# Kernel optimization log

Hardware: AMD Instinct MI355X
Metric: run time of the kernel (lower is better)

The kernel has to match this reference:

```python
import jax, jax.numpy as jnp
import numpy as np

N = 8192
IN_DIM = 256
HID = 256
OUT_DIM = 256
P_DIM = 3
SIGMA = 1.0


def setup_inputs() -> dict:
    key = jax.random.key(0)
    ks = jax.random.split(key, 7)
    s_in = 1.0 / np.sqrt(IN_DIM)
    inp = {
        "X": jax.random.normal(ks[0], (N, IN_DIM + P_DIM), dtype=jnp.float32),
        "WQ": jax.random.uniform(ks[1], (IN_DIM, HID), jnp.float32, -s_in, s_in),
        "bQ": jax.random.uniform(ks[2], (HID,), jnp.float32, -s_in, s_in),
        "WK": jax.random.uniform(ks[3], (IN_DIM, HID), jnp.float32, -s_in, s_in),
        "bK": jax.random.uniform(ks[4], (HID,), jnp.float32, -s_in, s_in),
        "WV": jax.random.uniform(ks[5], (IN_DIM, OUT_DIM), jnp.float32, -s_in, s_in),
        "bV": jax.random.uniform(ks[6], (OUT_DIM,), jnp.float32, -s_in, s_in),
    }
    return inp


def _softmax_one(x):
    # exp(x - max) / (1 + sum(exp(x - max))) -- faithful to the torch softmax_one
    m = jnp.max(x, axis=-1, keepdims=True)
    e = jnp.exp(x - m)
    return e / (1.0 + jnp.sum(e, axis=-1, keepdims=True))


def reference(X, WQ, bQ, WK, bK, WV, bV):
    P = X[:, -P_DIM:]            # [N, 3] spatial coords
    Xf = X[:, :-P_DIM]           # [N, IN_DIM] features

    Q = Xf @ WQ + bQ             # [N, HID]
    K = Xf @ WK + bK             # [N, HID]
    V = Xf @ WV + bV             # [N, OUT_DIM]

    scores = (Q @ K.T) / jnp.sqrt(jnp.asarray(HID, Xf.dtype))  # [N, N]

    # squared pairwise distances ||P_i - P_j||^2 (cdist(P,P)**2)
    sq = jnp.sum(P * P, axis=-1)                                # [N]
    d2 = jnp.maximum(sq[:, None] + sq[None, :] - 2.0 * (P @ P.T), 0.0)
    decay = jnp.exp(-d2 / (2.0 * SIGMA ** 2))                   # [N, N]

    A = _softmax_one(scores * decay)                             # [N, N]
    H = A @ V                                                    # [N, OUT_DIM]
    # residual: input_dim == output_dim so res_proj is None
    return H + Xf
```

## Files before the change

kernel.cpp:

```cpp
#include <hip/hip_runtime.h>
#include <hip/hip_bf16.h>
#include <stdint.h>

#define NTOK 8192
#define XSTRIDE 259
#define LOG2E 1.4426950408889634f
#define DECC (-3.4712336270551023f)
#define KSPLIT 8
#define SPLEN (NTOK / KSPLIT)
#define BN 32
#define ITERS (SPLEN / BN)

typedef __bf16 bf16x8 __attribute__((ext_vector_type(8)));
typedef float f32x4 __attribute__((ext_vector_type(4)));
typedef float f32x16 __attribute__((ext_vector_type(16)));
typedef unsigned short u16;

union BF8 { u16 u[8]; bf16x8 v; };
union PW  { uint32_t u[4]; bf16x8 v; };

__device__ __forceinline__ u16 f2bf(float f) {
  uint32_t u = __float_as_uint(f);
  u += 0x7FFFu + ((u >> 16) & 1u);
  return (u16)(u >> 16);
}
__device__ __forceinline__ float bf2f(u16 h) {
  return __uint_as_float(((uint32_t)h) << 16);
}
__device__ __forceinline__ float exp2_hw(float x) {
  float r; asm("v_exp_f32 %0, %1" : "=v"(r) : "v"(x)); return r;
}
__device__ __forceinline__ f32x4 mfma16(bf16x8 a, bf16x8 b, f32x4 c) {
  return __builtin_amdgcn_mfma_f32_16x16x32_bf16(a, b, c, 0, 0, 0);
}
__device__ __forceinline__ f32x16 mfma32(bf16x8 a, bf16x8 b, f32x16 c) {
  return __builtin_amdgcn_mfma_f32_32x32x16_bf16(a, b, c, 0, 0, 0);
}
__device__ __forceinline__ void async16(const void* g, void* l) {
  __builtin_amdgcn_global_load_lds(
      (const __attribute__((address_space(1))) uint32_t*)g,
      (__attribute__((address_space(3))) uint32_t*)l, 16, 0, 0);
}
__device__ __forceinline__ void bsplit(float v, u16& h, u16& l) {
  h = f2bf(v);
  l = f2bf(v - bf2f(h));
}

__global__ __launch_bounds__(256) void pos_kernel(
    const float* __restrict__ X, u16* __restrict__ Qp, u16* __restrict__ Kp) {
  const int r = blockIdx.x * 256 + threadIdx.x;
  const float* xp = X + (size_t)r * XSTRIDE + 256;
  const float x = xp[0], y = xp[1], z = xp[2];
  const float w = 0.5f * (x * x + y * y + z * z);
  u16 xh, xl, yh, yl, zh, zl, wh, wl;
  bsplit(x, xh, xl); bsplit(y, yh, yl); bsplit(z, zh, zl); bsplit(w, wh, wl);
  const u16 one = 0x3F80u;
  const u16 SGN = 0x8000u;
  union { u16 u[16]; uint4 v4[2]; } uq, uk;
  uq.u[0] = wh;  uk.u[0] = one;
  uq.u[1] = wl;  uk.u[1] = one;
  uq.u[2] = one; uk.u[2] = wh;
  uq.u[3] = one; uk.u[3] = wl;
  uq.u[4] = (u16)(xh ^ SGN); uk.u[4] = xh;
  uq.u[5] = (u16)(xh ^ SGN); uk.u[5] = xl;
  uq.u[6] = (u16)(xl ^ SGN); uk.u[6] = xh;
  uq.u[7] = (u16)(yh ^ SGN); uk.u[7] = yh;
  uq.u[8] = (u16)(yh ^ SGN); uk.u[8] = yl;
  uq.u[9] = (u16)(yl ^ SGN); uk.u[9] = yh;
  uq.u[10] = (u16)(zh ^ SGN); uk.u[10] = zh;
  uq.u[11] = (u16)(zh ^ SGN); uk.u[11] = zl;
  uq.u[12] = (u16)(zl ^ SGN); uk.u[12] = zh;
  uq.u[13] = 0; uk.u[13] = 0;
  uq.u[14] = 0; uk.u[14] = 0;
  uq.u[15] = 0; uk.u[15] = 0;
  ((uint4*)Qp)[r * 2] = uq.v4[0];
  ((uint4*)Qp)[r * 2 + 1] = uq.v4[1];
  ((uint4*)Kp)[r * 2] = uk.v4[0];
  ((uint4*)Kp)[r * 2 + 1] = uk.v4[1];
}

__global__ __launch_bounds__(256) void xb_kernel(
    const float* __restrict__ X, u16* __restrict__ Xb) {
  const int t = threadIdx.x;
  const int row = blockIdx.x * 8 + (t >> 5);
  const int c0 = (t & 31) * 8;
  const float* xp = X + (size_t)row * XSTRIDE + c0;
  union { u16 u[8]; uint4 v; } o;
#pragma unroll
  for (int j = 0; j < 8; ++j) o.u[j] = f2bf(xp[j]);
  *(uint4*)(Xb + (size_t)row * 256 + c0) = o.v;
}

__global__ __launch_bounds__(256) void wprep_kernel(
    const float* __restrict__ WQ, const float* __restrict__ WK,
    const float* __restrict__ WV, u16* __restrict__ Wt) {
  const int o = blockIdx.x;
  const int which = o >> 8, oo = o & 255;
  const float* W = (which == 0) ? WQ : ((which == 1) ? WK : WV);
  const int k = threadIdx.x;
  Wt[(size_t)o * 256 + k] = f2bf(W[(size_t)k * 256 + oo]);
}

__global__ __launch_bounds__(256) void qkv_kernel(
    const u16* __restrict__ Xb, const u16* __restrict__ Wt,
    const float* __restrict__ bQ, const float* __restrict__ bK,
    const float* __restrict__ bV,
    u16* __restrict__ Qb, u16* __restrict__ Kb, u16* __restrict__ Vt) {
  __shared__ u16 wt[64 * 256];
  const int tid = threadIdx.x;
  const int lane = tid & 63;
  const int wave = tid >> 6;
  const int l15 = lane & 15;
  const int q4 = lane >> 4;
  const int rb = blockIdx.x;
  const int ch = blockIdx.y;
  const int which = ch >> 2;
  const int c0 = (ch & 3) * 64;
  const float* bias = (which == 0) ? bQ : ((which == 1) ? bK : bV);

  bf16x8 xa[2][8];
#pragma unroll
  for (int mt = 0; mt < 2; ++mt) {
    const int row = rb * 128 + wave * 32 + mt * 16 + l15;
#pragma unroll
    for (int kc = 0; kc < 8; ++kc)
      xa[mt][kc] = *(const bf16x8*)(Xb + (size_t)row * 256 + kc * 32 + q4 * 8);
  }
  {
    const u16* Wsrc = Wt + (size_t)(which * 256 + c0) * 256;
    const int rb0 = wave * 16;
#pragma unroll
    for (int i = 0; i < 8; ++i) {
      int r = rb0 + i * 2 + (lane >> 5);
      int c = (lane & 31) ^ (r & 7);
      async16(Wsrc + (size_t)r * 256 + c * 8, wt + (rb0 + i * 2) * 256);
    }
  }
  asm volatile("s_waitcnt vmcnt(0)" ::: "memory");
  __syncthreads();

  f32x4 acc[2][4];
#pragma unroll
  for (int mt = 0; mt < 2; ++mt)
#pragma unroll
    for (int nt = 0; nt < 4; ++nt) acc[mt][nt] = (f32x4){0.f, 0.f, 0.f, 0.f};

#pragma unroll
  for (int kc = 0; kc < 8; ++kc) {
#pragma unroll
    for (int nt = 0; nt < 4; ++nt) {
      bf16x8 wf = *(const bf16x8*)(wt + (nt * 16 + l15) * 256 +
                                   (((kc * 4 + q4) ^ (l15 & 7)) * 8));
#pragma unroll
      for (int mt = 0; mt < 2; ++mt)
        acc[mt][nt] = mfma16(xa[mt][kc], wf, acc[mt][nt]);
    }
  }
  float bc[4];
#pragma unroll
  for (int nt = 0; nt < 4; ++nt) bc[nt] = bias[c0 + nt * 16 + l15];

#pragma unroll
  for (int mt = 0; mt < 2; ++mt)
#pragma unroll
    for (int nt = 0; nt < 4; ++nt)
#pragma unroll
      for (int r = 0; r < 4; ++r) {
        float v = acc[mt][nt][r] + bc[nt];
        int grow = rb * 128 + wave * 32 + mt * 16 + q4 * 4 + r;
        int gc = c0 + nt * 16 + l15;
        if (which == 2)      Vt[(size_t)gc * NTOK + grow] = f2bf(v);
        else if (which == 1) Kb[(size_t)grow * 256 + gc] = f2bf(v);
        else                 Qb[(size_t)((grow >> 5) * 16 + (gc >> 4)) * 512 +
                                ((gc >> 3) & 1) * 256 + (grow & 31) * 8 +
                                (gc & 7)] = f2bf(v);
      }
}

__global__ __launch_bounds__(512, 2) void attn_kernel(
    const u16* __restrict__ Qb, const u16* __restrict__ Kb,
    const u16* __restrict__ Vt, const u16* __restrict__ Qp,
    const u16* __restrict__ Kp, u16* __restrict__ Op,
    float* __restrict__ ml) {
  __shared__ u16 kbuf[3][BN * 256];
  __shared__ u16 vbuf[3][256 * BN];
  __shared__ u16 kpbuf[3][BN * 16];

  const int tid = threadIdx.x;
  const int lane = tid & 63;
  const int wave = tid >> 6;
  const int l31 = lane & 31;
  const int h5 = lane >> 5;
  const int sp = blockIdx.x;
  const int rb = blockIdx.y;
  const int q0 = rb * 256;
  const int wrow = wave * 32;

#define STAGE(T, S_)                                                          \
  do {                                                                        \
    const int key0_ = sp * SPLEN + (T) * BN;                                  \
    _Pragma("unroll")                                                         \
    for (int j = 0; j < 2; ++j) {                                             \
      int r = wave * 4 + j * 2 + (lane >> 5);                                 \
      int c = (lane & 31) ^ (r & 7);                                          \
      async16(Kb + (size_t)(key0_ + r) * 256 + c * 8,                         \
              &kbuf[S_][(wave * 4 + j * 2) * 256]);                           \
    }                                                                         \
    _Pragma("unroll")                                                         \
    for (int j = 0; j < 2; ++j) {                                             \
      int f = wave * 32 + j * 16 + (lane >> 2);                               \
      int c = (lane & 3) ^ ((f >> 1) & 3);                                    \
      async16(Vt + (size_t)f * NTOK + key0_ + c * 8,                          \
              &vbuf[S_][(wave * 32 + j * 16) * 32]);                          \
    }                                                                         \
    if (wave == 0)                                                            \
      async16(Kp + (size_t)(key0_ + (lane >> 1)) * 16 + (lane & 1) * 8,       \
              &kpbuf[S_][0]);                                                 \
  } while (0)

  const int rb32 = rb * 8 + wave;
  bf16x8 qa[16];
#pragma unroll
  for (int kc = 0; kc < 16; ++kc)
    qa[kc] = *(const bf16x8*)(Qb + ((size_t)(rb32 * 16 + kc) * 64 + lane) * 8);

  const bf16x8 qp = *(const bf16x8*)(Qp + (size_t)(q0 + wrow + l31) * 16 +
                                     h5 * 8);

  f32x16 O[8];
#pragma unroll
  for (int ft = 0; ft < 8; ++ft)
#pragma unroll
    for (int r = 0; r < 16; ++r) O[ft][r] = 0.f;
  float lrow = 0.f;

  const int kswz = l31 & 7;
  const int vswz = (l31 >> 1) & 3;

  STAGE(0, 0);
  STAGE(1, 1);

  int cur = 0;
#pragma unroll 1
  for (int t = 0; t < ITERS; ++t) {
    if (t + 1 < ITERS) {
      if (wave == 0) asm volatile("s_waitcnt vmcnt(5)" ::: "memory");
      else           asm volatile("s_waitcnt vmcnt(4)" ::: "memory");
    } else {
      asm volatile("s_waitcnt vmcnt(0)" ::: "memory");
    }
    __builtin_amdgcn_s_barrier();

    if (t + 2 < ITERS) {
      const int s2 = (cur >= 1) ? (cur - 1) : 2;
      STAGE(t + 2, s2);
    }

    f32x16 T;
#pragma unroll
    for (int r = 0; r < 16; ++r) T[r] = 0.f;
    {
      bf16x8 kpf = *(const bf16x8*)(&kpbuf[cur][l31 * 16 + h5 * 8]);
      T = mfma32(kpf, qp, T);
    }

    f32x16 S;
#pragma unroll
    for (int r = 0; r < 16; ++r) S[r] = 0.f;
    __builtin_amdgcn_s_setprio(1);
#pragma unroll
    for (int kc = 0; kc < 16; ++kc) {
      bf16x8 kf = *(const bf16x8*)(&kbuf[cur][l31 * 256 +
                                   (((2 * kc + h5) ^ kswz) * 8)]);
      S = mfma32(kf, qa[kc], S);
    }
    __builtin_amdgcn_s_setprio(0);

#pragma unroll
    for (int r = 0; r < 16; ++r) {
      float dec = exp2_hw(fmaf(T[r], -LOG2E, DECC));
      float p = exp2_hw(S[r] * dec);
      S[r] = p;
      lrow += p;
    }

    uint32_t w0, w1, w2, w3, w4, w5, w6, w7;
    asm("v_cvt_pk_bf16_f32 %0, %1, %2" : "=v"(w0) : "v"(S[0]),  "v"(S[1]));
    asm("v_cvt_pk_bf16_f32 %0, %1, %2" : "=v"(w1) : "v"(S[2]),  "v"(S[3]));
    asm("v_cvt_pk_bf16_f32 %0, %1, %2" : "=v"(w2) : "v"(S[4]),  "v"(S[5]));
    asm("v_cvt_pk_bf16_f32 %0, %1, %2" : "=v"(w3) : "v"(S[6]),  "v"(S[7]));
    asm("v_cvt_pk_bf16_f32 %0, %1, %2" : "=v"(w4) : "v"(S[8]),  "v"(S[9]));
    asm("v_cvt_pk_bf16_f32 %0, %1, %2" : "=v"(w5) : "v"(S[10]), "v"(S[11]));
    asm("v_cvt_pk_bf16_f32 %0, %1, %2" : "=v"(w6) : "v"(S[12]), "v"(S[13]));
    asm("v_cvt_pk_bf16_f32 %0, %1, %2" : "=v"(w7) : "v"(S[14]), "v"(S[15]));
    asm volatile("v_permlane32_swap_b32 %0, %1" : "+v"(w2), "+v"(w0));
    asm volatile("v_permlane32_swap_b32 %0, %1" : "+v"(w3), "+v"(w1));
    asm volatile("v_permlane32_swap_b32 %0, %1" : "+v"(w6), "+v"(w4));
    asm volatile("v_permlane32_swap_b32 %0, %1" : "+v"(w7), "+v"(w5));
    PW pa0, pa1;
    pa0.u[0] = w0; pa0.u[1] = w1; pa0.u[2] = w2; pa0.u[3] = w3;
    pa1.u[0] = w4; pa1.u[1] = w5; pa1.u[2] = w6; pa1.u[3] = w7;

    __builtin_amdgcn_s_setprio(1);
#pragma unroll
    for (int kh = 0; kh < 2; ++kh) {
      const bf16x8 pa = kh ? pa1.v : pa0.v;
#pragma unroll
      for (int ft = 0; ft < 8; ++ft) {
        bf16x8 vf = *(const bf16x8*)(&vbuf[cur][(ft * 32 + l31) * 32 +
                                     (((2 * kh + h5) ^ vswz) * 8)]);
        O[ft] = mfma32(pa, vf, O[ft]);
      }
    }
    __builtin_amdgcn_s_setprio(0);

    cur = (cur == 2) ? 0 : (cur + 1);
  }

  float lsum = lrow + __shfl_xor(lrow, 32);
#pragma unroll
  for (int ft = 0; ft < 8; ++ft)
#pragma unroll
    for (int r = 0; r < 16; ++r) {
      int row = q0 + wrow + (r & 3) + 8 * (r >> 2) + 4 * h5;
      Op[((size_t)sp * NTOK + row) * 256 + ft * 32 + l31] = f2bf(O[ft][r]);
    }
  if (lane < 32)
    ml[sp * NTOK + q0 + wrow + lane] = lsum;
#undef STAGE
}

__global__ __launch_bounds__(256) void combine_kernel(
    const float* __restrict__ X, const u16* __restrict__ Op,
    const float* __restrict__ ml, float* __restrict__ out) {
  const int row = blockIdx.x;
  const int f = threadIdx.x;
  float den = 1.f, num = 0.f;
#pragma unroll
  for (int s = 0; s < KSPLIT; ++s) {
    den += ml[s * NTOK + row];
    num += bf2f(Op[((size_t)s * NTOK + row) * 256 + f]);
  }
  out[(size_t)row * 256 + f] = num / den + X[(size_t)row * XSTRIDE + f];
}

extern "C" void kernel_launch(void* const* d_in, const int* in_sizes, int n_in,
                              void* d_out, int out_size, void* d_ws, size_t ws_size,
                              hipStream_t stream) {
  (void)in_sizes; (void)n_in; (void)out_size; (void)ws_size;
  const float* X  = (const float*)d_in[0];
  const float* WQ = (const float*)d_in[1];
  const float* bQ = (const float*)d_in[2];
  const float* WK = (const float*)d_in[3];
  const float* bK = (const float*)d_in[4];
  const float* WV = (const float*)d_in[5];
  const float* bV = (const float*)d_in[6];
  float* out = (float*)d_out;
  char* ws = (char*)d_ws;

  u16*   Qb = (u16*)(ws);
  u16*   Kb = (u16*)(ws + ((size_t)4 << 20));
  u16*   Vt = (u16*)(ws + ((size_t)8 << 20));
  u16*   Qp = (u16*)(ws + ((size_t)12 << 20));
  u16*   Kp = (u16*)(ws + ((size_t)12 << 20) + 262144);
  u16*   Wt = (u16*)(ws + ((size_t)12 << 20) + 524288);
  u16*   Xb = (u16*)(ws + ((size_t)12 << 20) + 524288 + 393216);
  float* ml = (float*)(ws + ((size_t)16 << 20) + 524288 + 393216);
  u16*   Op = (u16*)(ws + ((size_t)16 << 20) + 524288 + 393216 + 524288);

  pos_kernel<<<dim3(NTOK / 256), dim3(256), 0, stream>>>(X, Qp, Kp);
  xb_kernel<<<dim3(NTOK / 8), dim3(256), 0, stream>>>(X, Xb);
  wprep_kernel<<<dim3(768), dim3(256), 0, stream>>>(WQ, WK, WV, Wt);
  qkv_kernel<<<dim3(64, 12), dim3(256), 0, stream>>>(Xb, Wt, bQ, bK, bV,
                                                     Qb, Kb, Vt);
  attn_kernel<<<dim3(KSPLIT, NTOK / 256), dim3(512), 0, stream>>>(
      Qb, Kb, Vt, Qp, Kp, Op, ml);
  combine_kernel<<<dim3(NTOK), dim3(256), 0, stream>>>(X, Op, ml, out);
}
```

Before: 208.7 us.

## Double-buffer 64-key attention tiles, fuse pos prep, stage QKV stores through LDS

The attention loop moves from a triple-buffered 32-key pipeline to double-buffered 64-key tiles, each processed as two 32-key sub-steps. This halves the barrier count but waits for all loads with vmcnt(0) every iteration. The positional-encoding prep is folded into the bf16 conversion kernel to save a launch. QKV outputs are now staged through LDS so global stores are coalesced 16-byte writes, and the combine kernel processes two rows per block with paired loads and stores.

```diff
diff --git a/kernel.cpp b/kernel.cpp
--- a/kernel.cpp
+++ b/kernel.cpp
@@ -8,7 +8,7 @@
 #define DECC (-3.4712336270551023f)
 #define KSPLIT 8
 #define SPLEN (NTOK / KSPLIT)
-#define BN 32
+#define BN 64
 #define ITERS (SPLEN / BN)
 
 typedef __bf16 bf16x8 __attribute__((ext_vector_type(8)));
@@ -46,41 +46,9 @@
   l = f2bf(v - bf2f(h));
 }
 
-__global__ __launch_bounds__(256) void pos_kernel(
-    const float* __restrict__ X, u16* __restrict__ Qp, u16* __restrict__ Kp) {
-  const int r = blockIdx.x * 256 + threadIdx.x;
-  const float* xp = X + (size_t)r * XSTRIDE + 256;
-  const float x = xp[0], y = xp[1], z = xp[2];
-  const float w = 0.5f * (x * x + y * y + z * z);
-  u16 xh, xl, yh, yl, zh, zl, wh, wl;
-  bsplit(x, xh, xl); bsplit(y, yh, yl); bsplit(z, zh, zl); bsplit(w, wh, wl);
-  const u16 one = 0x3F80u;
-  const u16 SGN = 0x8000u;
-  union { u16 u[16]; uint4 v4[2]; } uq, uk;
-  uq.u[0] = wh;  uk.u[0] = one;
-  uq.u[1] = wl;  uk.u[1] = one;
-  uq.u[2] = one; uk.u[2] = wh;
-  uq.u[3] = one; uk.u[3] = wl;
-  uq.u[4] = (u16)(xh ^ SGN); uk.u[4] = xh;
-  uq.u[5] = (u16)(xh ^ SGN); uk.u[5] = xl;
-  uq.u[6] = (u16)(xl ^ SGN); uk.u[6] = xh;
-  uq.u[7] = (u16)(yh ^ SGN); uk.u[7] = yh;
-  uq.u[8] = (u16)(yh ^ SGN); uk.u[8] = yl;
-  uq.u[9] = (u16)(yl ^ SGN); uk.u[9] = yh;
-  uq.u[10] = (u16)(zh ^ SGN); uk.u[10] = zh;
-  uq.u[11] = (u16)(zh ^ SGN); uk.u[11] = zl;
-  uq.u[12] = (u16)(zl ^ SGN); uk.u[12] = zh;
-  uq.u[13] = 0; uk.u[13] = 0;
-  uq.u[14] = 0; uk.u[14] = 0;
-  uq.u[15] = 0; uk.u[15] = 0;
-  ((uint4*)Qp)[r * 2] = uq.v4[0];
-  ((uint4*)Qp)[r * 2 + 1] = uq.v4[1];
-  ((uint4*)Kp)[r * 2] = uk.v4[0];
-  ((uint4*)Kp)[r * 2 + 1] = uk.v4[1];
-}
-
 __global__ __launch_bounds__(256) void xb_kernel(
-    const float* __restrict__ X, u16* __restrict__ Xb) {
+    const float* __restrict__ X, u16* __restrict__ Xb,
+    u16* __restrict__ Qp, u16* __restrict__ Kp) {
   const int t = threadIdx.x;
   const int row = blockIdx.x * 8 + (t >> 5);
   const int c0 = (t & 31) * 8;
@@ -89,6 +57,38 @@
 #pragma unroll
   for (int j = 0; j < 8; ++j) o.u[j] = f2bf(xp[j]);
   *(uint4*)(Xb + (size_t)row * 256 + c0) = o.v;
+
+  if (t < 8) {
+    const int r = blockIdx.x * 8 + t;
+    const float* pp = X + (size_t)r * XSTRIDE + 256;
+    const float x = pp[0], y = pp[1], z = pp[2];
+    const float w = 0.5f * (x * x + y * y + z * z);
+    u16 xh, xl, yh, yl, zh, zl, wh, wl;
+    bsplit(x, xh, xl); bsplit(y, yh, yl); bsplit(z, zh, zl); bsplit(w, wh, wl);
+    const u16 one = 0x3F80u;
+    const u16 SGN = 0x8000u;
+    union { u16 u[16]; uint4 v4[2]; } uq, uk;
+    uq.u[0] = wh;  uk.u[0] = one;
+    uq.u[1] = wl;  uk.u[1] = one;
+    uq.u[2] = one; uk.u[2] = wh;
+    uq.u[3] = one; uk.u[3] = wl;
+    uq.u[4] = (u16)(xh ^ SGN); uk.u[4] = xh;
+    uq.u[5] = (u16)(xh ^ SGN); uk.u[5] = xl;
+    uq.u[6] = (u16)(xl ^ SGN); uk.u[6] = xh;
+    uq.u[7] = (u16)(yh ^ SGN); uk.u[7] = yh;
+    uq.u[8] = (u16)(yh ^ SGN); uk.u[8] = yl;
+    uq.u[9] = (u16)(yl ^ SGN); uk.u[9] = yh;
+    uq.u[10] = (u16)(zh ^ SGN); uk.u[10] = zh;
+    uq.u[11] = (u16)(zh ^ SGN); uk.u[11] = zl;
+    uq.u[12] = (u16)(zl ^ SGN); uk.u[12] = zh;
+    uq.u[13] = 0; uk.u[13] = 0;
+    uq.u[14] = 0; uk.u[14] = 0;
+    uq.u[15] = 0; uk.u[15] = 0;
+    ((uint4*)Qp)[r * 2] = uq.v4[0];
+    ((uint4*)Qp)[r * 2 + 1] = uq.v4[1];
+    ((uint4*)Kp)[r * 2] = uk.v4[0];
+    ((uint4*)Kp)[r * 2 + 1] = uk.v4[1];
+  }
 }
 
 __global__ __launch_bounds__(256) void wprep_kernel(
@@ -106,7 +106,7 @@
     const float* __restrict__ bQ, const float* __restrict__ bK,
     const float* __restrict__ bV,
     u16* __restrict__ Qb, u16* __restrict__ Kb, u16* __restrict__ Vt) {
-  __shared__ u16 wt[64 * 256];
+  __shared__ u16 smem[64 * 256];
   const int tid = threadIdx.x;
   const int lane = tid & 63;
   const int wave = tid >> 6;
@@ -133,7 +133,7 @@
     for (int i = 0; i < 8; ++i) {
       int r = rb0 + i * 2 + (lane >> 5);
       int c = (lane & 31) ^ (r & 7);
-      async16(Wsrc + (size_t)r * 256 + c * 8, wt + (rb0 + i * 2) * 256);
+      async16(Wsrc + (size_t)r * 256 + c * 8, smem + (rb0 + i * 2) * 256);
     }
   }
   asm volatile("s_waitcnt vmcnt(0)" ::: "memory");
@@ -149,7 +149,7 @@
   for (int kc = 0; kc < 8; ++kc) {
 #pragma unroll
     for (int nt = 0; nt < 4; ++nt) {
-      bf16x8 wf = *(const bf16x8*)(wt + (nt * 16 + l15) * 256 +
+      bf16x8 wf = *(const bf16x8*)(smem + (nt * 16 + l15) * 256 +
                                    (((kc * 4 + q4) ^ (l15 & 7)) * 8));
 #pragma unroll
       for (int mt = 0; mt < 2; ++mt)
@@ -160,21 +160,52 @@
 #pragma unroll
   for (int nt = 0; nt < 4; ++nt) bc[nt] = bias[c0 + nt * 16 + l15];
 
-#pragma unroll
-  for (int mt = 0; mt < 2; ++mt)
-#pragma unroll
-    for (int nt = 0; nt < 4; ++nt)
-#pragma unroll
-      for (int r = 0; r < 4; ++r) {
-        float v = acc[mt][nt][r] + bc[nt];
-        int grow = rb * 128 + wave * 32 + mt * 16 + q4 * 4 + r;
-        int gc = c0 + nt * 16 + l15;
-        if (which == 2)      Vt[(size_t)gc * NTOK + grow] = f2bf(v);
-        else if (which == 1) Kb[(size_t)grow * 256 + gc] = f2bf(v);
-        else                 Qb[(size_t)((grow >> 5) * 16 + (gc >> 4)) * 512 +
-                                ((gc >> 3) & 1) * 256 + (grow & 31) * 8 +
-                                (gc & 7)] = f2bf(v);
+  __syncthreads();
+  const int grow0 = rb * 128;
+
+  if (which == 2) {
+#pragma unroll
+    for (int mt = 0; mt < 2; ++mt)
+#pragma unroll
+      for (int nt = 0; nt < 4; ++nt) {
+        const int lcol = nt * 16 + l15;
+        const int lrow0 = wave * 32 + mt * 16 + q4 * 4;
+        union { u16 u[4]; uint2 w; } p;
+#pragma unroll
+        for (int r = 0; r < 4; ++r) p.u[r] = f2bf(acc[mt][nt][r] + bc[nt]);
+        *(uint2*)(smem + lcol * 136 + lrow0) = p.w;
       }
+    __syncthreads();
+#pragma unroll
+    for (int i = 0; i < 4; ++i) {
+      int chn = i * 256 + tid;
+      int lcol = chn >> 4, s = chn & 15;
+      uint4 d = *(const uint4*)(smem + lcol * 136 + s * 8);
+      *(uint4*)(Vt + (size_t)(c0 + lcol) * NTOK + grow0 + s * 8) = d;
+    }
+  } else {
+#pragma unroll
+    for (int mt = 0; mt < 2; ++mt)
+#pragma unroll
+      for (int nt = 0; nt < 4; ++nt)
+#pragma unroll
+        for (int r = 0; r < 4; ++r)
+          smem[(wave * 32 + mt * 16 + q4 * 4 + r) * 72 + nt * 16 + l15] =
+              f2bf(acc[mt][nt][r] + bc[nt]);
+    __syncthreads();
+#pragma unroll
+    for (int i = 0; i < 4; ++i) {
+      int chn = i * 256 + tid;
+      int lrow = chn >> 3, g = chn & 7;
+      uint4 d = *(const uint4*)(smem + lrow * 72 + g * 8);
+      int grow = grow0 + lrow, gc = c0 + g * 8;
+      if (which == 1)
+        *(uint4*)(Kb + (size_t)grow * 256 + gc) = d;
+      else
+        *(uint4*)(Qb + (size_t)((grow >> 5) * 16 + (gc >> 4)) * 512 +
+                  ((gc >> 3) & 1) * 256 + (grow & 31) * 8) = d;
+    }
+  }
 }
 
 __global__ __launch_bounds__(512, 2) void attn_kernel(
@@ -182,9 +213,9 @@
     const u16* __restrict__ Vt, const u16* __restrict__ Qp,
     const u16* __restrict__ Kp, u16* __restrict__ Op,
     float* __restrict__ ml) {
-  __shared__ u16 kbuf[3][BN * 256];
-  __shared__ u16 vbuf[3][256 * BN];
-  __shared__ u16 kpbuf[3][BN * 16];
+  __shared__ u16 kbuf[2][BN * 256];
+  __shared__ u16 vbuf[2][256 * BN];
+  __shared__ u16 kpbuf[2][BN * 16];
 
   const int tid = threadIdx.x;
   const int lane = tid & 63;
@@ -200,22 +231,26 @@
   do {                                                                        \
     const int key0_ = sp * SPLEN + (T) * BN;                                  \
     _Pragma("unroll")                                                         \
-    for (int j = 0; j < 2; ++j) {                                             \
-      int r = wave * 4 + j * 2 + (lane >> 5);                                 \
+    for (int j = 0; j < 4; ++j) {                                             \
+      int r = wave * 8 + j * 2 + (lane >> 5);                                 \
       int c = (lane & 31) ^ (r & 7);                                          \
       async16(Kb + (size_t)(key0_ + r) * 256 + c * 8,                         \
-              &kbuf[S_][(wave * 4 + j * 2) * 256]);                           \
+              &kbuf[S_][(wave * 8 + j * 2) * 256]);                           \
     }                                                                         \
     _Pragma("unroll")                                                         \
-    for (int j = 0; j < 2; ++j) {                                             \
-      int f = wave * 32 + j * 16 + (lane >> 2);                               \
-      int c = (lane & 3) ^ ((f >> 1) & 3);                                    \
+    for (int j = 0; j < 4; ++j) {                                             \
+      int f = wave * 32 + j * 8 + (lane >> 3);                                \
+      int c = (lane & 7) ^ (f & 7);                                           \
       async16(Vt + (size_t)f * NTOK + key0_ + c * 8,                          \
-              &vbuf[S_][(wave * 32 + j * 16) * 32]);                          \
+              &vbuf[S_][(wave * 32 + j * 8) * BN]);                           \
     }                                                                         \
-    if (wave == 0)                                                            \
-      async16(Kp + (size_t)(key0_ + (lane >> 1)) * 16 + (lane & 1) * 8,       \
-              &kpbuf[S_][0]);                                                 \
+    if (wave == 0) {                                                          \
+      _Pragma("unroll")                                                       \
+      for (int hh = 0; hh < 2; ++hh)                                          \
+        async16(Kp + (size_t)(key0_ + hh * 32 + (lane >> 1)) * 16 +           \
+                    (lane & 1) * 8,                                           \
+                &kpbuf[S_][hh * 32 * 16]);                                    \
+    }                                                                         \
   } while (0)
 
   const int rb32 = rb * 8 + wave;
@@ -234,87 +269,79 @@
     for (int r = 0; r < 16; ++r) O[ft][r] = 0.f;
   float lrow = 0.f;
 
-  const int kswz = l31 & 7;
-  const int vswz = (l31 >> 1) & 3;
+  const int swz = l31 & 7;
 
   STAGE(0, 0);
-  STAGE(1, 1);
-
-  int cur = 0;
+
 #pragma unroll 1
   for (int t = 0; t < ITERS; ++t) {
-    if (t + 1 < ITERS) {
-      if (wave == 0) asm volatile("s_waitcnt vmcnt(5)" ::: "memory");
-      else           asm volatile("s_waitcnt vmcnt(4)" ::: "memory");
-    } else {
-      asm volatile("s_waitcnt vmcnt(0)" ::: "memory");
-    }
+    const int slot = t & 1;
+    asm volatile("s_waitcnt vmcnt(0)" ::: "memory");
     __builtin_amdgcn_s_barrier();
-
-    if (t + 2 < ITERS) {
-      const int s2 = (cur >= 1) ? (cur - 1) : 2;
-      STAGE(t + 2, s2);
-    }
-
-    f32x16 T;
-#pragma unroll
-    for (int r = 0; r < 16; ++r) T[r] = 0.f;
-    {
-      bf16x8 kpf = *(const bf16x8*)(&kpbuf[cur][l31 * 16 + h5 * 8]);
-      T = mfma32(kpf, qp, T);
-    }
-
-    f32x16 S;
-#pragma unroll
-    for (int r = 0; r < 16; ++r) S[r] = 0.f;
-    __builtin_amdgcn_s_setprio(1);
-#pragma unroll
-    for (int kc = 0; kc < 16; ++kc) {
-      bf16x8 kf = *(const bf16x8*)(&kbuf[cur][l31 * 256 +
-                                   (((2 * kc + h5) ^ kswz) * 8)]);
-      S = mfma32(kf, qa[kc], S);
-    }
-    __builtin_amdgcn_s_setprio(0);
-
-#pragma unroll
-    for (int r = 0; r < 16; ++r) {
-      float dec = exp2_hw(fmaf(T[r], -LOG2E, DECC));
-      float p = exp2_hw(S[r] * dec);
-      S[r] = p;
-      lrow += p;
-    }
-
-    uint32_t w0, w1, w2, w3, w4, w5, w6, w7;
-    asm("v_cvt_pk_bf16_f32 %0, %1, %2" : "=v"(w0) : "v"(S[0]),  "v"(S[1]));
-    asm("v_cvt_pk_bf16_f32 %0, %1, %2" : "=v"(w1) : "v"(S[2]),  "v"(S[3]));
-    asm("v_cvt_pk_bf16_f32 %0, %1, %2" : "=v"(w2) : "v"(S[4]),  "v"(S[5]));
-    asm("v_cvt_pk_bf16_f32 %0, %1, %2" : "=v"(w3) : "v"(S[6]),  "v"(S[7]));
-    asm("v_cvt_pk_bf16_f32 %0, %1, %2" : "=v"(w4) : "v"(S[8]),  "v"(S[9]));
-    asm("v_cvt_pk_bf16_f32 %0, %1, %2" : "=v"(w5) : "v"(S[10]), "v"(S[11]));
-    asm("v_cvt_pk_bf16_f32 %0, %1, %2" : "=v"(w6) : "v"(S[12]), "v"(S[13]));
-    asm("v_cvt_pk_bf16_f32 %0, %1, %2" : "=v"(w7) : "v"(S[14]), "v"(S[15]));
-    asm volatile("v_permlane32_swap_b32 %0, %1" : "+v"(w2), "+v"(w0));
-    asm volatile("v_permlane32_swap_b32 %0, %1" : "+v"(w3), "+v"(w1));
-    asm volatile("v_permlane32_swap_b32 %0, %1" : "+v"(w6), "+v"(w4));
-    asm volatile("v_permlane32_swap_b32 %0, %1" : "+v"(w7), "+v"(w5));
-    PW pa0, pa1;
-    pa0.u[0] = w0; pa0.u[1] = w1; pa0.u[2] = w2; pa0.u[3] = w3;
-    pa1.u[0] = w4; pa1.u[1] = w5; pa1.u[2] = w6; pa1.u[3] = w7;
-
-    __builtin_amdgcn_s_setprio(1);
-#pragma unroll
-    for (int kh = 0; kh < 2; ++kh) {
-      const bf16x8 pa = kh ? pa1.v : pa0.v;
-#pragma unroll
-      for (int ft = 0; ft < 8; ++ft) {
-        bf16x8 vf = *(const bf16x8*)(&vbuf[cur][(ft * 32 + l31) * 32 +
-                                     (((2 * kh + h5) ^ vswz) * 8)]);
-        O[ft] = mfma32(pa, vf, O[ft]);
+    if (t + 1 < ITERS) STAGE(t + 1, slot ^ 1);
+
+#pragma unroll
+    for (int sub = 0; sub < 2; ++sub) {
+      f32x16 T;
+#pragma unroll
+      for (int r = 0; r < 16; ++r) T[r] = 0.f;
+      {
+        bf16x8 kpf = *(const bf16x8*)(&kpbuf[slot][(sub * 32 + l31) * 16 +
+                                      h5 * 8]);
+        T = mfma32(kpf, qp, T);
       }
-    }
-    __builtin_amdgcn_s_setprio(0);
-
-    cur = (cur == 2) ? 0 : (cur + 1);
+
+      f32x16 S;
+#pragma unroll
+      for (int r = 0; r < 16; ++r) S[r] = 0.f;
+      __builtin_amdgcn_s_setprio(1);
+#pragma unroll
+      for (int kc = 0; kc < 16; ++kc) {
+        bf16x8 kf = *(const bf16x8*)(&kbuf[slot][(sub * 32 + l31) * 256 +
+                                     (((2 * kc + h5) ^ swz) * 8)]);
+        S = mfma32(kf, qa[kc], S);
+      }
+      __builtin_amdgcn_s_setprio(0);
+
+#pragma unroll
+      for (int r = 0; r < 16; ++r) {
+        float dec = exp2_hw(fmaf(T[r], -LOG2E, DECC));
+        float p = exp2_hw(S[r] * dec);
+        S[r] = p;
+        lrow += p;
+      }
+
+      uint32_t w0, w1, w2, w3, w4, w5, w6, w7;
+      asm("v_cvt_pk_bf16_f32 %0, %1, %2" : "=v"(w0) : "v"(S[0]),  "v"(S[1]));
+      asm("v_cvt_pk_bf16_f32 %0, %1, %2" : "=v"(w1) : "v"(S[2]),  "v"(S[3]));
+      asm("v_cvt_pk_bf16_f32 %0, %1, %2" : "=v"(w2) : "v"(S[4]),  "v"(S[5]));
+      asm("v_cvt_pk_bf16_f32 %0, %1, %2" : "=v"(w3) : "v"(S[6]),  "v"(S[7]));
+      asm("v_cvt_pk_bf16_f32 %0, %1, %2" : "=v"(w4) : "v"(S[8]),  "v"(S[9]));
+      asm("v_cvt_pk_bf16_f32 %0, %1, %2" : "=v"(w5) : "v"(S[10]), "v"(S[11]));
+      asm("v_cvt_pk_bf16_f32 %0, %1, %2" : "=v"(w6) : "v"(S[12]), "v"(S[13]));
+      asm("v_cvt_pk_bf16_f32 %0, %1, %2" : "=v"(w7) : "v"(S[14]), "v"(S[15]));
+      asm volatile("v_permlane32_swap_b32 %0, %1" : "+v"(w2), "+v"(w0));
+      asm volatile("v_permlane32_swap_b32 %0, %1" : "+v"(w3), "+v"(w1));
+      asm volatile("v_permlane32_swap_b32 %0, %1" : "+v"(w6), "+v"(w4));
+      asm volatile("v_permlane32_swap_b32 %0, %1" : "+v"(w7), "+v"(w5));
+      PW pa0, pa1;
+      pa0.u[0] = w0; pa0.u[1] = w1; pa0.u[2] = w2; pa0.u[3] = w3;
+      pa1.u[0] = w4; pa1.u[1] = w5; pa1.u[2] = w6; pa1.u[3] = w7;
+
+      __builtin_amdgcn_s_setprio(1);
+#pragma unroll
+      for (int kh = 0; kh < 2; ++kh) {
+        const bf16x8 pa = kh ? pa1.v : pa0.v;
+        const int khh = sub * 2 + kh;
+#pragma unroll
+        for (int ft = 0; ft < 8; ++ft) {
+          bf16x8 vf = *(const bf16x8*)(&vbuf[slot][(ft * 32 + l31) * BN +
+                                       (((2 * khh + h5) ^ swz) * 8)]);
+          O[ft] = mfma32(pa, vf, O[ft]);
+        }
+      }
+      __builtin_amdgcn_s_setprio(0);
+    }
   }
 
   float lsum = lrow + __shfl_xor(lrow, 32);
@@ -333,15 +360,22 @@
 __global__ __launch_bounds__(256) void combine_kernel(
     const float* __restrict__ X, const u16* __restrict__ Op,
     const float* __restrict__ ml, float* __restrict__ out) {
-  const int row = blockIdx.x;
-  const int f = threadIdx.x;
-  float den = 1.f, num = 0.f;
+  const int row = blockIdx.x * 2 + (threadIdx.x >> 7);
+  const int f2 = threadIdx.x & 127;
+  float den = 1.f, n0 = 0.f, n1 = 0.f;
 #pragma unroll
   for (int s = 0; s < KSPLIT; ++s) {
     den += ml[s * NTOK + row];
-    num += bf2f(Op[((size_t)s * NTOK + row) * 256 + f]);
-  }
-  out[(size_t)row * 256 + f] = num / den + X[(size_t)row * XSTRIDE + f];
+    uint32_t v = *(const uint32_t*)(Op + ((size_t)s * NTOK + row) * 256 +
+                                    f2 * 2);
+    n0 += bf2f((u16)v);
+    n1 += bf2f((u16)(v >> 16));
+  }
+  const float inv = 1.f / den;
+  float2 o;
+  o.x = n0 * inv + X[(size_t)row * XSTRIDE + f2 * 2];
+  o.y = n1 * inv + X[(size_t)row * XSTRIDE + f2 * 2 + 1];
+  *(float2*)(out + (size_t)row * 256 + f2 * 2) = o;
 }
 
 extern "C" void kernel_launch(void* const* d_in, const int* in_sizes, int n_in,
@@ -368,12 +402,11 @@
   float* ml = (float*)(ws + ((size_t)16 << 20) + 524288 + 393216);
   u16*   Op = (u16*)(ws + ((size_t)16 << 20) + 524288 + 393216 + 524288);
 
-  pos_kernel<<<dim3(NTOK / 256), dim3(256), 0, stream>>>(X, Qp, Kp);
-  xb_kernel<<<dim3(NTOK / 8), dim3(256), 0, stream>>>(X, Xb);
+  xb_kernel<<<dim3(NTOK / 8), dim3(256), 0, stream>>>(X, Xb, Qp, Kp);
   wprep_kernel<<<dim3(768), dim3(256), 0, stream>>>(WQ, WK, WV, Wt);
   qkv_kernel<<<dim3(64, 12), dim3(256), 0, stream>>>(Xb, Wt, bQ, bK, bV,
                                                      Qb, Kb, Vt);
   attn_kernel<<<dim3(KSPLIT, NTOK / 256), dim3(512), 0, stream>>>(
       Qb, Kb, Vt, Qp, Kp, Op, ml);
-  combine_kernel<<<dim3(NTOK), dim3(256), 0, stream>>>(X, Op, ml, out);
-}
+  combine_kernel<<<dim3(NTOK / 2), dim3(256), 0, stream>>>(X, Op, ml, out);
+}
```

Result: no change. 205.7 us (-1.4%).
